# Optimization experiments

Measured on AMD Instinct MI355X. Metric: run time of the kernel, lower is better.

## Reference

```python
import jax, jax.numpy as jnp
import numpy as np

HEADS = 16
DIM_HEAD = 64
SCALE = DIM_HEAD ** -0.5
LN_EPS = 1e-5


def setup_inputs() -> dict:
    key = jax.random.key(0)
    ks = jax.random.split(key, 4)
    B, N, D = 2, 2048, 1024
    inner = HEADS * DIM_HEAD  # 1024
    x = jax.random.normal(ks[0], (B, N, D), dtype=jnp.float32)
    m = jax.random.normal(ks[1], (B, N, N), dtype=jnp.float32)
    gamma = jnp.ones((D,), dtype=jnp.float32)
    beta = jnp.zeros((D,), dtype=jnp.float32)
    W_qkv = jax.random.normal(ks[2], (D, 3 * inner), dtype=jnp.float32) * (D ** -0.5)
    W_out = jax.random.normal(ks[3], (inner, D), dtype=jnp.float32) * (inner ** -0.5)
    return {"x": x, "m": m, "gamma": gamma, "beta": beta, "W_qkv": W_qkv, "W_out": W_out}


def reference(x, m, gamma, beta, W_qkv, W_out):
    B, N, D = x.shape
    # LayerNorm
    mu = jnp.mean(x, axis=-1, keepdims=True)
    var = jnp.var(x, axis=-1, keepdims=True)
    xn = (x - mu) * jax.lax.rsqrt(var + LN_EPS) * gamma + beta
    # QKV projection (no bias)
    qkv = xn @ W_qkv  # [B, N, 3*inner]
    q, k, v = jnp.split(qkv, 3, axis=-1)
    split_heads = lambda t: t.reshape(B, N, HEADS, DIM_HEAD).transpose(0, 2, 1, 3)  # b h n d
    q, k, v = split_heads(q), split_heads(k), split_heads(v)
    # Non-standard order: mask added BEFORE scaling
    qk = jnp.einsum('bhid,bhjd->bhij', q, k)
    dots = (qk + m[:, None, :, :]) * SCALE
    attn = jax.nn.softmax(dots, axis=-1)
    out = jnp.einsum('bhij,bhjd->bhid', attn, v)
    out = out.transpose(0, 2, 1, 3).reshape(B, N, HEADS * DIM_HEAD)
    return out @ W_out  # dropout is identity at inference
```

## Files before the change

kernel.cpp:

```cpp
#include <hip/hip_runtime.h>
#include <hip/hip_bf16.h>
#include <math.h>

typedef _Float16 f16;
typedef _Float16 f16x4 __attribute__((ext_vector_type(4)));
typedef _Float16 f16x8 __attribute__((ext_vector_type(8)));
typedef float f32x4 __attribute__((ext_vector_type(4)));

#define HD 64
#define NH 16
#define BATCH 2
#define SEQ 2048
#define DMODEL 1024
#define NQKV 3072
#define ROWS 4096
#define NEG_BIG (-1.0e30f)
#define SCALE_LOG2E 0.18033688011112042f

__device__ __forceinline__ f32x4 mfma16h(f16x8 a, f16x8 b, f32x4 c){
  return __builtin_amdgcn_mfma_f32_16x16x32_f16(a, b, c, 0, 0, 0);
}

__device__ __forceinline__ void gload16(const f16* g, f16* l){
  __builtin_amdgcn_global_load_lds(
      (const __attribute__((address_space(1))) unsigned int*)(g),
      (__attribute__((address_space(3))) unsigned int*)(l), 16, 0, 0);
}

__global__ __launch_bounds__(256) void ln_kernel(const float* __restrict__ x,
    const float* __restrict__ gamma, const float* __restrict__ beta,
    f16* __restrict__ xn)
{
  int row = blockIdx.x;
  int tid = threadIdx.x;
  float4 v = ((const float4*)(x + (size_t)row * DMODEL))[tid];
  float s  = v.x + v.y + v.z + v.w;
  float s2 = v.x*v.x + v.y*v.y + v.z*v.z + v.w*v.w;
  #pragma unroll
  for (int off = 32; off; off >>= 1){ s += __shfl_xor(s, off); s2 += __shfl_xor(s2, off); }
  __shared__ float red[8];
  int wave = tid >> 6, lane = tid & 63;
  if (lane == 0){ red[wave] = s; red[4 + wave] = s2; }
  __syncthreads();
  s  = red[0] + red[1] + red[2] + red[3];
  s2 = red[4] + red[5] + red[6] + red[7];
  float mu  = s * (1.f / DMODEL);
  float var = s2 * (1.f / DMODEL) - mu * mu;
  float rs  = rsqrtf(var + 1e-5f);
  float4 g  = ((const float4*)gamma)[tid];
  float4 be = ((const float4*)beta)[tid];
  f16x4 o;
  o[0] = (f16)((v.x - mu) * rs * g.x + be.x);
  o[1] = (f16)((v.y - mu) * rs * g.y + be.y);
  o[2] = (f16)((v.z - mu) * rs * g.z + be.z);
  o[3] = (f16)((v.w - mu) * rs * g.w + be.w);
  *(f16x4*)(xn + (size_t)row * DMODEL + tid*4) = o;
}

__global__ __launch_bounds__(256) void transpose_f2h_kernel(const float* __restrict__ in,
    f16* __restrict__ out, int R, int C)
{
  __shared__ float t[32][33];
  int c0 = blockIdx.x * 32, r0 = blockIdx.y * 32;
  int lx = threadIdx.x & 31, ly = threadIdx.x >> 5;
  #pragma unroll
  for (int i = 0; i < 32; i += 8) t[ly + i][lx] = in[(size_t)(r0 + ly + i) * C + c0 + lx];
  __syncthreads();
  #pragma unroll
  for (int i = 0; i < 32; i += 8) out[(size_t)(c0 + ly + i) * R + r0 + lx] = (f16)t[lx][ly + i];
}

__global__ __launch_bounds__(256, 3) void gemm_qkv(const f16* __restrict__ A,
    const f16* __restrict__ Bt, f16* __restrict__ Qo, f16* __restrict__ Ko,
    f16* __restrict__ Vo)
{
  __shared__ __align__(16) f16 As[2][128][32];
  __shared__ __align__(16) f16 Bs[2][128][32];
  const int K = DMODEL;
  int bm = blockIdx.y * 128, bn = blockIdx.x * 128;
  int tid = threadIdx.x;
  int wave = tid >> 6, lane = tid & 63, quad = lane >> 4, l15 = lane & 15;
  int mw = (wave >> 1) * 64, nw = (wave & 1) * 64;

  int sr0 = wave*16 + (lane >> 2);
  int sr1 = sr0 + 64;
  int sc  = (lane & 3) ^ (sr0 & 3);
  const f16* Ag = A  + (size_t)bm * K;
  const f16* Bg = Bt + (size_t)bn * K;
  f16* ldsA0 = &As[0][wave*16     ][0];
  f16* ldsA1 = &As[0][wave*16 + 64][0];
  f16* ldsB0 = &Bs[0][wave*16     ][0];
  f16* ldsB1 = &Bs[0][wave*16 + 64][0];

#define QSTAGE(buf, k0) do{ \
    gload16(Ag + (size_t)sr0 * K + (k0) + sc*8, ldsA0 + (buf)*4096); \
    gload16(Ag + (size_t)sr1 * K + (k0) + sc*8, ldsA1 + (buf)*4096); \
    gload16(Bg + (size_t)sr0 * K + (k0) + sc*8, ldsB0 + (buf)*4096); \
    gload16(Bg + (size_t)sr1 * K + (k0) + sc*8, ldsB1 + (buf)*4096); }while(0)

  f32x4 zero = {0.f, 0.f, 0.f, 0.f};
  f32x4 acc[4][4];
  #pragma unroll
  for (int i = 0; i < 4; i++)
    #pragma unroll
    for (int j = 0; j < 4; j++) acc[i][j] = zero;

  QSTAGE(0, 0);
  const int NS = K / 32;
  for (int it = 0; it < NS; ++it){
    int cur = it & 1;
    asm volatile("s_waitcnt vmcnt(0)" ::: "memory");
    __syncthreads();
    if (it + 1 < NS) QSTAGE(cur ^ 1, (it + 1) * 32);
    int ca = (quad ^ (l15 & 3)) * 8;
    f16x8 af[4], bfr[4];
    #pragma unroll
    for (int i = 0; i < 4; i++) af[i]  = *(const f16x8*)&As[cur][mw + i*16 + l15][ca];
    #pragma unroll
    for (int i = 0; i < 4; i++) bfr[i] = *(const f16x8*)&Bs[cur][nw + i*16 + l15][ca];
    __builtin_amdgcn_s_setprio(1);
    #pragma unroll
    for (int mi = 0; mi < 4; mi++)
      #pragma unroll
      for (int ni = 0; ni < 4; ni++)
        acc[mi][ni] = mfma16h(af[mi], bfr[ni], acc[mi][ni]);
    __builtin_amdgcn_s_setprio(0);
  }
#undef QSTAGE

  #pragma unroll
  for (int mi = 0; mi < 4; mi++){
    #pragma unroll
    for (int ni = 0; ni < 4; ni++){
      int c = bn + nw + ni*16 + l15;
      int which = c >> 10;
      int hc = c & 1023;
      int h = hc >> 6, d = hc & 63;
      if (which == 2){
        int r = bm + mw + mi*16 + quad*4;
        int b = r >> 11, nseq = r & 2047;
        size_t bh = (size_t)(b * NH + h);
        f16x4 vv;
        #pragma unroll
        for (int reg = 0; reg < 4; reg++) vv[reg] = (f16)acc[mi][ni][reg];
        *(f16x4*)(Vo + (bh * HD + d) * SEQ + nseq) = vv;
      } else {
        #pragma unroll
        for (int reg = 0; reg < 4; reg++){
          int r = bm + mw + mi*16 + quad*4 + reg;
          float v = acc[mi][ni][reg];
          int b = r >> 11, nseq = r & 2047;
          size_t bh = (size_t)(b * NH + h);
          if (which == 0) Qo[(bh * SEQ + nseq) * HD + d] = (f16)v;
          else            Ko[(bh * SEQ + nseq) * HD + d] = (f16)v;
        }
      }
    }
  }
}

__global__ __launch_bounds__(256, 4) void gemm_out(const f16* __restrict__ A,
    const f16* __restrict__ Bt, float* __restrict__ C, int M, int N, int K)
{
  __shared__ __align__(16) f16 As[2][64][32];
  __shared__ __align__(16) f16 Bs[2][128][32];
  int bm = blockIdx.y * 64, bn = blockIdx.x * 128;
  int tid = threadIdx.x;
  int wave = tid >> 6, lane = tid & 63, quad = lane >> 4, l15 = lane & 15;
  int mw = (wave >> 1) * 32, nw = (wave & 1) * 64;

  int sr0 = wave*16 + (lane >> 2);
  int sc  = (lane & 3) ^ (sr0 & 3);
  const f16* Ag = A  + (size_t)bm * K;
  const f16* Bg = Bt + (size_t)bn * K;
  f16* ldsA0 = &As[0][wave*16     ][0];
  f16* ldsB0 = &Bs[0][wave*16     ][0];
  f16* ldsB1 = &Bs[0][wave*16 + 64][0];

#define OSTAGE(buf, k0) do{ \
    gload16(Ag + (size_t)sr0 * K + (k0) + sc*8, ldsA0 + (buf)*2048); \
    gload16(Bg + (size_t)sr0 * K + (k0) + sc*8, ldsB0 + (buf)*4096); \
    gload16(Bg + (size_t)(sr0 + 64) * K + (k0) + sc*8, ldsB1 + (buf)*4096); }while(0)

  f32x4 zero = {0.f, 0.f, 0.f, 0.f};
  f32x4 acc[2][4];
  #pragma unroll
  for (int i = 0; i < 2; i++)
    #pragma unroll
    for (int j = 0; j < 4; j++) acc[i][j] = zero;

  OSTAGE(0, 0);
  const int NS = DMODEL / 32;
  for (int it = 0; it < NS; ++it){
    int cur = it & 1;
    asm volatile("s_waitcnt vmcnt(0)" ::: "memory");
    __syncthreads();
    if (it + 1 < NS) OSTAGE(cur ^ 1, (it + 1) * 32);
    int ca = (quad ^ (l15 & 3)) * 8;
    f16x8 af[2], bfr[4];
    #pragma unroll
    for (int i = 0; i < 2; i++) af[i]  = *(const f16x8*)&As[cur][mw + i*16 + l15][ca];
    #pragma unroll
    for (int i = 0; i < 4; i++) bfr[i] = *(const f16x8*)&Bs[cur][nw + i*16 + l15][ca];
    __builtin_amdgcn_s_setprio(1);
    #pragma unroll
    for (int mi = 0; mi < 2; mi++)
      #pragma unroll
      for (int ni = 0; ni < 4; ni++)
        acc[mi][ni] = mfma16h(af[mi], bfr[ni], acc[mi][ni]);
    __builtin_amdgcn_s_setprio(0);
  }
#undef OSTAGE

  #pragma unroll
  for (int mi = 0; mi < 2; mi++)
    #pragma unroll
    for (int ni = 0; ni < 4; ni++)
      #pragma unroll
      for (int reg = 0; reg < 4; reg++){
        int r = bm + mw + mi*16 + quad*4 + reg;
        int c = bn + nw + ni*16 + l15;
        C[(size_t)r * N + c] = acc[mi][ni][reg];
      }
}

__global__ __launch_bounds__(256, 4) void attn_kernel(const f16* __restrict__ Q,
    const f16* __restrict__ Kb, const f16* __restrict__ Vt,
    const float* __restrict__ mask, f16* __restrict__ Ao)
{
  __shared__ __align__(16) f16 KsB[2][64*64];
  __shared__ __align__(16) f16 VsB[2][64*64];
  __shared__ __align__(16) f16 Ps[4*16*64];

  int bh = blockIdx.y; int b = bh >> 4; int h = bh & 15;
  int q0 = blockIdx.x * 64;
  int tid = threadIdx.x;
  int wave = tid >> 6, lane = tid & 63, quad = lane >> 4, l15 = lane & 15;

  int rA = (wave*2 + 0)*8 + (lane >> 3);
  int rB = (wave*2 + 1)*8 + (lane >> 3);
  int cp = lane & 7;
  int ccA = cp ^ (rA & 7);
  int ccB = cp ^ (rB & 7);
  const f16* Kg = Kb + (size_t)bh * SEQ * HD;
  const f16* Vg = Vt + (size_t)bh * HD * SEQ;
  f16* ldsKA = &KsB[0][0] + (wave*2 + 0)*8*64;
  f16* ldsKB = &KsB[0][0] + (wave*2 + 1)*8*64;
  f16* ldsVA = &VsB[0][0] + (wave*2 + 0)*8*64;
  f16* ldsVB = &VsB[0][0] + (wave*2 + 1)*8*64;

  f16x8 qf[2];
  {
    const f16* qrow = Q + ((size_t)bh * SEQ + q0 + wave*16 + l15) * HD + quad*8;
    qf[0] = *(const f16x8*)(qrow);
    qf[1] = *(const f16x8*)(qrow + 32);
  }

  const float* mrow = mask + ((size_t)b * SEQ + q0 + wave*16 + l15) * SEQ + quad*4;

  gload16(Kg + (size_t)(0 + rA)*HD + ccA*8, ldsKA);
  gload16(Kg + (size_t)(0 + rB)*HD + ccB*8, ldsKB);
  gload16(Vg + (size_t)rA*SEQ + 0 + ccA*8, ldsVA);
  gload16(Vg + (size_t)rB*SEQ + 0 + ccB*8, ldsVB);

  f32x4 zero = {0.f, 0.f, 0.f, 0.f};
  f32x4 O[4];
  #pragma unroll
  for (int nt = 0; nt < 4; nt++) O[nt] = zero;
  float mrun = NEG_BIG, lrun = 0.f;

  const int NT = SEQ / 64;
  for (int it = 0; it < NT; ++it){
    int cur = it & 1;
    int j0 = it * 64;
    asm volatile("s_waitcnt vmcnt(0)" ::: "memory");
    __syncthreads();
    if (it + 1 < NT){
      int nb = cur ^ 1;
      int j0n = j0 + 64;
      gload16(Kg + (size_t)(j0n + rA)*HD + ccA*8, ldsKA + nb*4096);
      gload16(Kg + (size_t)(j0n + rB)*HD + ccB*8, ldsKB + nb*4096);
      gload16(Vg + (size_t)rA*SEQ + j0n + ccA*8, ldsVA + nb*4096);
      gload16(Vg + (size_t)rB*SEQ + j0n + ccB*8, ldsVB + nb*4096);
    }
    const f16* Ksc = &KsB[cur][0];
    const f16* Vsc = &VsB[cur][0];

    float sv[4][4];
    __builtin_amdgcn_s_setprio(1);
    #pragma unroll
    for (int jt = 0; jt < 4; jt++){
      f32x4 a = zero;
      int r = jt*16 + l15;
      #pragma unroll
      for (int kk = 0; kk < 2; kk++){
        f16x8 kf = *(const f16x8*)&Ksc[r*64 + (((kk*4 + quad) ^ (r & 7))*8)];
        a = mfma16h(kf, qf[kk], a);
      }
      float4 mv = *(const float4*)(mrow + j0 + jt*16);
      sv[jt][0] = (a[0] + mv.x) * SCALE_LOG2E;
      sv[jt][1] = (a[1] + mv.y) * SCALE_LOG2E;
      sv[jt][2] = (a[2] + mv.z) * SCALE_LOG2E;
      sv[jt][3] = (a[3] + mv.w) * SCALE_LOG2E;
    }
    __builtin_amdgcn_s_setprio(0);

    float m0 = fmaxf(fmaxf(sv[0][0], sv[0][1]), fmaxf(sv[0][2], sv[0][3]));
    float m1 = fmaxf(fmaxf(sv[1][0], sv[1][1]), fmaxf(sv[1][2], sv[1][3]));
    float m2 = fmaxf(fmaxf(sv[2][0], sv[2][1]), fmaxf(sv[2][2], sv[2][3]));
    float m3 = fmaxf(fmaxf(sv[3][0], sv[3][1]), fmaxf(sv[3][2], sv[3][3]));
    float tmax = fmaxf(fmaxf(m0, m1), fmaxf(m2, m3));
    tmax = fmaxf(tmax, __shfl_xor(tmax, 16));
    tmax = fmaxf(tmax, __shfl_xor(tmax, 32));

    if (__any(tmax > mrun + 8.f)){
      float nm = fmaxf(mrun, tmax);
      float alpha = exp2f(mrun - nm);
      mrun = nm;
      lrun *= alpha;
      float aR[4];
      #pragma unroll
      for (int reg = 0; reg < 4; reg++)
        aR[reg] = __shfl(alpha, (lane & 48) | (quad*4 + reg));
      #pragma unroll
      for (int nt = 0; nt < 4; nt++)
        #pragma unroll
        for (int reg = 0; reg < 4; reg++) O[nt][reg] *= aR[reg];
    }

    float ps = 0.f;
    #pragma unroll
    for (int jt = 0; jt < 4; jt++)
      #pragma unroll
      for (int reg = 0; reg < 4; reg++){
        float p = exp2f(sv[jt][reg] - mrun);
        sv[jt][reg] = p; ps += p;
      }
    lrun += ps;

    #pragma unroll
    for (int jt = 0; jt < 4; jt++){
      f16x4 ph;
      ph[0] = (f16)sv[jt][0]; ph[1] = (f16)sv[jt][1];
      ph[2] = (f16)sv[jt][2]; ph[3] = (f16)sv[jt][3];
      *(f16x4*)&Ps[wave*1024 + l15*64 + (((jt*2 + (quad>>1)) ^ (l15 & 7))*8) + (quad & 1)*4] = ph;
    }

    __builtin_amdgcn_s_setprio(1);
    #pragma unroll
    for (int nt = 0; nt < 4; nt++){
      #pragma unroll
      for (int kk = 0; kk < 2; kk++){
        int rv = nt*16 + l15;
        f16x8 pf = *(const f16x8*)&Ps[wave*1024 + l15*64 + (((kk*4 + quad) ^ (l15 & 7))*8)];
        f16x8 vf = *(const f16x8*)&Vsc[rv*64 + (((kk*4 + quad) ^ (rv & 7))*8)];
        O[nt] = mfma16h(pf, vf, O[nt]);
      }
    }
    __builtin_amdgcn_s_setprio(0);
  }

  lrun += __shfl_xor(lrun, 16);
  lrun += __shfl_xor(lrun, 32);
  float lR[4];
  #pragma unroll
  for (int reg = 0; reg < 4; reg++)
    lR[reg] = __shfl(lrun, (lane & 48) | (quad*4 + reg));
  #pragma unroll
  for (int nt = 0; nt < 4; nt++){
    #pragma unroll
    for (int reg = 0; reg < 4; reg++){
      float o = O[nt][reg] / lR[reg];
      int r = q0 + wave*16 + quad*4 + reg;
      Ao[((size_t)(b * SEQ + r)) * DMODEL + h * HD + nt*16 + l15] = (f16)o;
    }
  }
}

extern "C" void kernel_launch(void* const* d_in, const int* in_sizes, int n_in,
                              void* d_out, int out_size, void* d_ws, size_t ws_size,
                              hipStream_t stream)
{
  (void)in_sizes; (void)n_in; (void)out_size; (void)ws_size;
  const float* x     = (const float*)d_in[0];
  const float* m     = (const float*)d_in[1];
  const float* gamma = (const float*)d_in[2];
  const float* beta  = (const float*)d_in[3];
  const float* Wqkv  = (const float*)d_in[4];
  const float* Wout  = (const float*)d_in[5];
  float* out = (float*)d_out;

  char* ws = (char*)d_ws;
  f16* xn    = (f16*)(ws + 0);
  f16* Ao    = (f16*)(ws + 0);
  f16* Qb    = (f16*)(ws + 8388608);
  f16* WoutT = (f16*)(ws + 8388608);
  f16* Kbuf  = (f16*)(ws + 16777216);
  f16* Vtb   = (f16*)(ws + 25165824);
  f16* WqkvT = (f16*)(ws + 33554432);

  ln_kernel<<<ROWS, 256, 0, stream>>>(x, gamma, beta, xn);
  transpose_f2h_kernel<<<dim3(NQKV/32, DMODEL/32), 256, 0, stream>>>(Wqkv, WqkvT, DMODEL, NQKV);
  gemm_qkv<<<dim3(NQKV/128, ROWS/128), 256, 0, stream>>>(xn, WqkvT, Qb, Kbuf, Vtb);
  attn_kernel<<<dim3(SEQ/64, BATCH*NH), 256, 0, stream>>>(Qb, Kbuf, Vtb, m, Ao);
  transpose_f2h_kernel<<<dim3(DMODEL/32, DMODEL/32), 256, 0, stream>>>(Wout, WoutT, DMODEL, DMODEL);
  gemm_out<<<dim3(DMODEL/128, ROWS/64), 256, 0, stream>>>(Ao, WoutT, out, ROWS, DMODEL, DMODEL);
}
```

Before: 253.1 us.

## Process 128 query rows per attention block, two 16-row tiles per wave

Each wave now handles two 16-row query tiles, so the block covers 128 queries and the grid halves. K and V fragments loaded from LDS are reused across both tiles, which halves K/V global and LDS traffic per query. The mask loads are hoisted ahead of the QK MFMAs. In exchange, register pressure roughly doubles (launch bounds lowered to 2 blocks per CU), the grid shrinks to 512 blocks, and occupancy drops.

```diff
diff --git a/kernel.cpp b/kernel.cpp
--- a/kernel.cpp
+++ b/kernel.cpp
@@ -224,16 +224,16 @@
       }
 }
 
-__global__ __launch_bounds__(256, 4) void attn_kernel(const f16* __restrict__ Q,
+__global__ __launch_bounds__(256, 2) void attn_kernel(const f16* __restrict__ Q,
     const f16* __restrict__ Kb, const f16* __restrict__ Vt,
     const float* __restrict__ mask, f16* __restrict__ Ao)
 {
   __shared__ __align__(16) f16 KsB[2][64*64];
   __shared__ __align__(16) f16 VsB[2][64*64];
-  __shared__ __align__(16) f16 Ps[4*16*64];
+  __shared__ __align__(16) f16 Ps[8*16*64];
 
   int bh = blockIdx.y; int b = bh >> 4; int h = bh & 15;
-  int q0 = blockIdx.x * 64;
+  int q0 = blockIdx.x * 128;
   int tid = threadIdx.x;
   int wave = tid >> 6, lane = tid & 63, quad = lane >> 4, l15 = lane & 15;
 
@@ -249,14 +249,18 @@
   f16* ldsVA = &VsB[0][0] + (wave*2 + 0)*8*64;
   f16* ldsVB = &VsB[0][0] + (wave*2 + 1)*8*64;
 
-  f16x8 qf[2];
-  {
-    const f16* qrow = Q + ((size_t)bh * SEQ + q0 + wave*16 + l15) * HD + quad*8;
-    qf[0] = *(const f16x8*)(qrow);
-    qf[1] = *(const f16x8*)(qrow + 32);
-  }
-
-  const float* mrow = mask + ((size_t)b * SEQ + q0 + wave*16 + l15) * SEQ + quad*4;
+  f16x8 qf[2][2];
+  #pragma unroll
+  for (int u = 0; u < 2; u++){
+    const f16* qrow = Q + ((size_t)bh * SEQ + q0 + wave*32 + u*16 + l15) * HD + quad*8;
+    qf[u][0] = *(const f16x8*)(qrow);
+    qf[u][1] = *(const f16x8*)(qrow + 32);
+  }
+
+  const float* mrow[2];
+  #pragma unroll
+  for (int u = 0; u < 2; u++)
+    mrow[u] = mask + ((size_t)b * SEQ + q0 + wave*32 + u*16 + l15) * SEQ + quad*4;
 
   gload16(Kg + (size_t)(0 + rA)*HD + ccA*8, ldsKA);
   gload16(Kg + (size_t)(0 + rB)*HD + ccB*8, ldsKB);
@@ -264,10 +268,12 @@
   gload16(Vg + (size_t)rB*SEQ + 0 + ccB*8, ldsVB);
 
   f32x4 zero = {0.f, 0.f, 0.f, 0.f};
-  f32x4 O[4];
-  #pragma unroll
-  for (int nt = 0; nt < 4; nt++) O[nt] = zero;
-  float mrun = NEG_BIG, lrun = 0.f;
+  f32x4 O[2][4];
+  #pragma unroll
+  for (int u = 0; u < 2; u++)
+    #pragma unroll
+    for (int nt = 0; nt < 4; nt++) O[u][nt] = zero;
+  float mrun[2] = {NEG_BIG, NEG_BIG}, lrun[2] = {0.f, 0.f};
 
   const int NT = SEQ / 64;
   for (int it = 0; it < NT; ++it){
@@ -286,93 +292,117 @@
     const f16* Ksc = &KsB[cur][0];
     const f16* Vsc = &VsB[cur][0];
 
-    float sv[4][4];
+    float4 mc[2][4];
+    #pragma unroll
+    for (int u = 0; u < 2; u++)
+      #pragma unroll
+      for (int jt = 0; jt < 4; jt++)
+        mc[u][jt] = *(const float4*)(mrow[u] + j0 + jt*16);
+
+    float sv[2][4][4];
     __builtin_amdgcn_s_setprio(1);
     #pragma unroll
     for (int jt = 0; jt < 4; jt++){
-      f32x4 a = zero;
       int r = jt*16 + l15;
-      #pragma unroll
-      for (int kk = 0; kk < 2; kk++){
-        f16x8 kf = *(const f16x8*)&Ksc[r*64 + (((kk*4 + quad) ^ (r & 7))*8)];
-        a = mfma16h(kf, qf[kk], a);
-      }
-      float4 mv = *(const float4*)(mrow + j0 + jt*16);
-      sv[jt][0] = (a[0] + mv.x) * SCALE_LOG2E;
-      sv[jt][1] = (a[1] + mv.y) * SCALE_LOG2E;
-      sv[jt][2] = (a[2] + mv.z) * SCALE_LOG2E;
-      sv[jt][3] = (a[3] + mv.w) * SCALE_LOG2E;
+      f16x8 kf0 = *(const f16x8*)&Ksc[r*64 + (((0 + quad) ^ (r & 7))*8)];
+      f16x8 kf1 = *(const f16x8*)&Ksc[r*64 + (((4 + quad) ^ (r & 7))*8)];
+      #pragma unroll
+      for (int u = 0; u < 2; u++){
+        f32x4 a = zero;
+        a = mfma16h(kf0, qf[u][0], a);
+        a = mfma16h(kf1, qf[u][1], a);
+        sv[u][jt][0] = (a[0] + mc[u][jt].x) * SCALE_LOG2E;
+        sv[u][jt][1] = (a[1] + mc[u][jt].y) * SCALE_LOG2E;
+        sv[u][jt][2] = (a[2] + mc[u][jt].z) * SCALE_LOG2E;
+        sv[u][jt][3] = (a[3] + mc[u][jt].w) * SCALE_LOG2E;
+      }
     }
     __builtin_amdgcn_s_setprio(0);
 
-    float m0 = fmaxf(fmaxf(sv[0][0], sv[0][1]), fmaxf(sv[0][2], sv[0][3]));
-    float m1 = fmaxf(fmaxf(sv[1][0], sv[1][1]), fmaxf(sv[1][2], sv[1][3]));
-    float m2 = fmaxf(fmaxf(sv[2][0], sv[2][1]), fmaxf(sv[2][2], sv[2][3]));
-    float m3 = fmaxf(fmaxf(sv[3][0], sv[3][1]), fmaxf(sv[3][2], sv[3][3]));
-    float tmax = fmaxf(fmaxf(m0, m1), fmaxf(m2, m3));
-    tmax = fmaxf(tmax, __shfl_xor(tmax, 16));
-    tmax = fmaxf(tmax, __shfl_xor(tmax, 32));
-
-    if (__any(tmax > mrun + 8.f)){
-      float nm = fmaxf(mrun, tmax);
-      float alpha = exp2f(mrun - nm);
-      mrun = nm;
-      lrun *= alpha;
-      float aR[4];
-      #pragma unroll
-      for (int reg = 0; reg < 4; reg++)
-        aR[reg] = __shfl(alpha, (lane & 48) | (quad*4 + reg));
-      #pragma unroll
-      for (int nt = 0; nt < 4; nt++)
+    #pragma unroll
+    for (int u = 0; u < 2; u++){
+      float m0 = fmaxf(fmaxf(sv[u][0][0], sv[u][0][1]), fmaxf(sv[u][0][2], sv[u][0][3]));
+      float m1 = fmaxf(fmaxf(sv[u][1][0], sv[u][1][1]), fmaxf(sv[u][1][2], sv[u][1][3]));
+      float m2 = fmaxf(fmaxf(sv[u][2][0], sv[u][2][1]), fmaxf(sv[u][2][2], sv[u][2][3]));
+      float m3 = fmaxf(fmaxf(sv[u][3][0], sv[u][3][1]), fmaxf(sv[u][3][2], sv[u][3][3]));
+      float tmax = fmaxf(fmaxf(m0, m1), fmaxf(m2, m3));
+      tmax = fmaxf(tmax, __shfl_xor(tmax, 16));
+      tmax = fmaxf(tmax, __shfl_xor(tmax, 32));
+
+      if (__any(tmax > mrun[u] + 8.f)){
+        float nm = fmaxf(mrun[u], tmax);
+        float alpha = exp2f(mrun[u] - nm);
+        mrun[u] = nm;
+        lrun[u] *= alpha;
+        float aR[4];
         #pragma unroll
-        for (int reg = 0; reg < 4; reg++) O[nt][reg] *= aR[reg];
-    }
-
-    float ps = 0.f;
-    #pragma unroll
-    for (int jt = 0; jt < 4; jt++)
+        for (int reg = 0; reg < 4; reg++)
+          aR[reg] = __shfl(alpha, (lane & 48) | (quad*4 + reg));
+        #pragma unroll
+        for (int nt = 0; nt < 4; nt++)
+          #pragma unroll
+          for (int reg = 0; reg < 4; reg++) O[u][nt][reg] *= aR[reg];
+      }
+
+      float ps = 0.f;
+      #pragma unroll
+      for (int jt = 0; jt < 4; jt++)
+        #pragma unroll
+        for (int reg = 0; reg < 4; reg++){
+          float p = exp2f(sv[u][jt][reg] - mrun[u]);
+          sv[u][jt][reg] = p; ps += p;
+        }
+      lrun[u] += ps;
+
+      #pragma unroll
+      for (int jt = 0; jt < 4; jt++){
+        f16x4 ph;
+        ph[0] = (f16)sv[u][jt][0]; ph[1] = (f16)sv[u][jt][1];
+        ph[2] = (f16)sv[u][jt][2]; ph[3] = (f16)sv[u][jt][3];
+        *(f16x4*)&Ps[wave*2048 + u*1024 + l15*64
+                     + (((jt*2 + (quad>>1)) ^ (l15 & 7))*8) + (quad & 1)*4] = ph;
+      }
+    }
+
+    f16x8 pf[2][2];
+    #pragma unroll
+    for (int u = 0; u < 2; u++)
+      #pragma unroll
+      for (int kk = 0; kk < 2; kk++)
+        pf[u][kk] = *(const f16x8*)&Ps[wave*2048 + u*1024 + l15*64
+                                       + (((kk*4 + quad) ^ (l15 & 7))*8)];
+    __builtin_amdgcn_s_setprio(1);
+    #pragma unroll
+    for (int nt = 0; nt < 4; nt++){
+      int rv = nt*16 + l15;
+      f16x8 vf0 = *(const f16x8*)&Vsc[rv*64 + (((0 + quad) ^ (rv & 7))*8)];
+      f16x8 vf1 = *(const f16x8*)&Vsc[rv*64 + (((4 + quad) ^ (rv & 7))*8)];
+      #pragma unroll
+      for (int u = 0; u < 2; u++){
+        O[u][nt] = mfma16h(pf[u][0], vf0, O[u][nt]);
+        O[u][nt] = mfma16h(pf[u][1], vf1, O[u][nt]);
+      }
+    }
+    __builtin_amdgcn_s_setprio(0);
+  }
+
+  #pragma unroll
+  for (int u = 0; u < 2; u++){
+    float l = lrun[u];
+    l += __shfl_xor(l, 16);
+    l += __shfl_xor(l, 32);
+    float lR[4];
+    #pragma unroll
+    for (int reg = 0; reg < 4; reg++)
+      lR[reg] = __shfl(l, (lane & 48) | (quad*4 + reg));
+    #pragma unroll
+    for (int nt = 0; nt < 4; nt++){
       #pragma unroll
       for (int reg = 0; reg < 4; reg++){
-        float p = exp2f(sv[jt][reg] - mrun);
-        sv[jt][reg] = p; ps += p;
-      }
-    lrun += ps;
-
-    #pragma unroll
-    for (int jt = 0; jt < 4; jt++){
-      f16x4 ph;
-      ph[0] = (f16)sv[jt][0]; ph[1] = (f16)sv[jt][1];
-      ph[2] = (f16)sv[jt][2]; ph[3] = (f16)sv[jt][3];
-      *(f16x4*)&Ps[wave*1024 + l15*64 + (((jt*2 + (quad>>1)) ^ (l15 & 7))*8) + (quad & 1)*4] = ph;
-    }
-
-    __builtin_amdgcn_s_setprio(1);
-    #pragma unroll
-    for (int nt = 0; nt < 4; nt++){
-      #pragma unroll
-      for (int kk = 0; kk < 2; kk++){
-        int rv = nt*16 + l15;
-        f16x8 pf = *(const f16x8*)&Ps[wave*1024 + l15*64 + (((kk*4 + quad) ^ (l15 & 7))*8)];
-        f16x8 vf = *(const f16x8*)&Vsc[rv*64 + (((kk*4 + quad) ^ (rv & 7))*8)];
-        O[nt] = mfma16h(pf, vf, O[nt]);
-      }
-    }
-    __builtin_amdgcn_s_setprio(0);
-  }
-
-  lrun += __shfl_xor(lrun, 16);
-  lrun += __shfl_xor(lrun, 32);
-  float lR[4];
-  #pragma unroll
-  for (int reg = 0; reg < 4; reg++)
-    lR[reg] = __shfl(lrun, (lane & 48) | (quad*4 + reg));
-  #pragma unroll
-  for (int nt = 0; nt < 4; nt++){
-    #pragma unroll
-    for (int reg = 0; reg < 4; reg++){
-      float o = O[nt][reg] / lR[reg];
-      int r = q0 + wave*16 + quad*4 + reg;
-      Ao[((size_t)(b * SEQ + r)) * DMODEL + h * HD + nt*16 + l15] = (f16)o;
+        float o = O[u][nt][reg] / lR[reg];
+        int r = q0 + wave*32 + u*16 + quad*4 + reg;
+        Ao[((size_t)(b * SEQ + r)) * DMODEL + h * HD + nt*16 + l15] = (f16)o;
+      }
     }
   }
 }
@@ -402,7 +432,7 @@
   ln_kernel<<<ROWS, 256, 0, stream>>>(x, gamma, beta, xn);
   transpose_f2h_kernel<<<dim3(NQKV/32, DMODEL/32), 256, 0, stream>>>(Wqkv, WqkvT, DMODEL, NQKV);
   gemm_qkv<<<dim3(NQKV/128, ROWS/128), 256, 0, stream>>>(xn, WqkvT, Qb, Kbuf, Vtb);
-  attn_kernel<<<dim3(SEQ/64, BATCH*NH), 256, 0, stream>>>(Qb, Kbuf, Vtb, m, Ao);
+  attn_kernel<<<dim3(SEQ/128, BATCH*NH), 256, 0, stream>>>(Qb, Kbuf, Vtb, m, Ao);
   transpose_f2h_kernel<<<dim3(DMODEL/32, DMODEL/32), 256, 0, stream>>>(Wout, WoutT, DMODEL, DMODEL);
   gemm_out<<<dim3(DMODEL/128, ROWS/64), 256, 0, stream>>>(Ao, WoutT, out, ROWS, DMODEL, DMODEL);
 }
```

Result: slower. 258.5 us (+2.2%).

## Rewrite attention with 32x32 MFMA tiles, register-resident P via permlane swap

Applied to the files above, without the earlier changes.

The attention kernel now processes 128 query rows per block (32 per wave) using 32x32x16 MFMA instructions. The softmax probabilities are repacked in registers with permlane32_swap instead of a round trip through LDS. The softmax scale is folded into Q inside the QKV GEMM epilogue, so only the mask needs an FMA with the scale. The output is staged through an LDS slab so global stores are 16-byte and coalesced. This halves the grid and raises register use (launch bound lowered to 2 blocks per CU), which risks lower occupancy in exchange for more reuse of each K/V tile.

```diff
diff --git a/kernel.cpp b/kernel.cpp
--- a/kernel.cpp
+++ b/kernel.cpp
@@ -3,9 +3,12 @@
 #include <math.h>
 
 typedef _Float16 f16;
+typedef __fp16 hf2 __attribute__((ext_vector_type(2)));
 typedef _Float16 f16x4 __attribute__((ext_vector_type(4)));
 typedef _Float16 f16x8 __attribute__((ext_vector_type(8)));
 typedef float f32x4 __attribute__((ext_vector_type(4)));
+typedef float f32x16 __attribute__((ext_vector_type(16)));
+typedef unsigned int u32x2 __attribute__((ext_vector_type(2)));
 
 #define HD 64
 #define NH 16
@@ -19,6 +22,16 @@
 
 __device__ __forceinline__ f32x4 mfma16h(f16x8 a, f16x8 b, f32x4 c){
   return __builtin_amdgcn_mfma_f32_16x16x32_f16(a, b, c, 0, 0, 0);
+}
+__device__ __forceinline__ f32x16 mfma32h(f16x8 a, f16x8 b, f32x16 c){
+  return __builtin_amdgcn_mfma_f32_32x32x16_f16(a, b, c, 0, 0, 0);
+}
+__device__ __forceinline__ u32x2 pswap(unsigned a, unsigned b){
+  return __builtin_amdgcn_permlane32_swap(a, b, false, false);
+}
+__device__ __forceinline__ unsigned pk16(float a, float b){
+  hf2 r = __builtin_amdgcn_cvt_pkrtz(a, b);
+  return __builtin_bit_cast(unsigned, r);
 }
 
 __device__ __forceinline__ void gload16(const f16* g, f16* l){
@@ -151,7 +164,7 @@
           float v = acc[mi][ni][reg];
           int b = r >> 11, nseq = r & 2047;
           size_t bh = (size_t)(b * NH + h);
-          if (which == 0) Qo[(bh * SEQ + nseq) * HD + d] = (f16)v;
+          if (which == 0) Qo[(bh * SEQ + nseq) * HD + d] = (f16)(v * SCALE_LOG2E);
           else            Ko[(bh * SEQ + nseq) * HD + d] = (f16)v;
         }
       }
@@ -224,18 +237,19 @@
       }
 }
 
-__global__ __launch_bounds__(256, 4) void attn_kernel(const f16* __restrict__ Q,
+__global__ __launch_bounds__(256, 2) void attn_kernel(const f16* __restrict__ Q,
     const f16* __restrict__ Kb, const f16* __restrict__ Vt,
     const float* __restrict__ mask, f16* __restrict__ Ao)
 {
   __shared__ __align__(16) f16 KsB[2][64*64];
   __shared__ __align__(16) f16 VsB[2][64*64];
-  __shared__ __align__(16) f16 Ps[4*16*64];
+  __shared__ __align__(16) f16 Ob[4][32*72];
 
   int bh = blockIdx.y; int b = bh >> 4; int h = bh & 15;
-  int q0 = blockIdx.x * 64;
+  int q0 = blockIdx.x * 128;
   int tid = threadIdx.x;
-  int wave = tid >> 6, lane = tid & 63, quad = lane >> 4, l15 = lane & 15;
+  int wave = tid >> 6, lane = tid & 63;
+  int l31 = lane & 31, hi = lane >> 5;
 
   int rA = (wave*2 + 0)*8 + (lane >> 3);
   int rB = (wave*2 + 1)*8 + (lane >> 3);
@@ -249,24 +263,23 @@
   f16* ldsVA = &VsB[0][0] + (wave*2 + 0)*8*64;
   f16* ldsVB = &VsB[0][0] + (wave*2 + 1)*8*64;
 
-  f16x8 qf[2];
+  f16x8 qb[4];
   {
-    const f16* qrow = Q + ((size_t)bh * SEQ + q0 + wave*16 + l15) * HD + quad*8;
-    qf[0] = *(const f16x8*)(qrow);
-    qf[1] = *(const f16x8*)(qrow + 32);
-  }
-
-  const float* mrow = mask + ((size_t)b * SEQ + q0 + wave*16 + l15) * SEQ + quad*4;
+    const f16* qrow = Q + ((size_t)bh * SEQ + q0 + wave*32 + l31) * HD + hi*8;
+    #pragma unroll
+    for (int kt = 0; kt < 4; kt++) qb[kt] = *(const f16x8*)(qrow + kt*16);
+  }
+
+  const float* mrow = mask + ((size_t)b * SEQ + q0 + wave*32 + l31) * SEQ;
 
   gload16(Kg + (size_t)(0 + rA)*HD + ccA*8, ldsKA);
   gload16(Kg + (size_t)(0 + rB)*HD + ccB*8, ldsKB);
   gload16(Vg + (size_t)rA*SEQ + 0 + ccA*8, ldsVA);
   gload16(Vg + (size_t)rB*SEQ + 0 + ccB*8, ldsVB);
 
-  f32x4 zero = {0.f, 0.f, 0.f, 0.f};
-  f32x4 O[4];
-  #pragma unroll
-  for (int nt = 0; nt < 4; nt++) O[nt] = zero;
+  f32x16 O0, O1;
+  #pragma unroll
+  for (int i = 0; i < 16; i++){ O0[i] = 0.f; O1[i] = 0.f; }
   float mrun = NEG_BIG, lrun = 0.f;
 
   const int NT = SEQ / 64;
@@ -286,94 +299,129 @@
     const f16* Ksc = &KsB[cur][0];
     const f16* Vsc = &VsB[cur][0];
 
-    float sv[4][4];
+    float4 mv0[4], mv1[4];
+    #pragma unroll
+    for (int g = 0; g < 4; g++){
+      mv0[g] = *(const float4*)(mrow + j0 +      g*8 + hi*4);
+      mv1[g] = *(const float4*)(mrow + j0 + 32 + g*8 + hi*4);
+    }
+
+    f32x16 s0, s1;
+    #pragma unroll
+    for (int i = 0; i < 16; i++){ s0[i] = 0.f; s1[i] = 0.f; }
     __builtin_amdgcn_s_setprio(1);
     #pragma unroll
-    for (int jt = 0; jt < 4; jt++){
-      f32x4 a = zero;
-      int r = jt*16 + l15;
-      #pragma unroll
-      for (int kk = 0; kk < 2; kk++){
-        f16x8 kf = *(const f16x8*)&Ksc[r*64 + (((kk*4 + quad) ^ (r & 7))*8)];
-        a = mfma16h(kf, qf[kk], a);
-      }
-      float4 mv = *(const float4*)(mrow + j0 + jt*16);
-      sv[jt][0] = (a[0] + mv.x) * SCALE_LOG2E;
-      sv[jt][1] = (a[1] + mv.y) * SCALE_LOG2E;
-      sv[jt][2] = (a[2] + mv.z) * SCALE_LOG2E;
-      sv[jt][3] = (a[3] + mv.w) * SCALE_LOG2E;
+    for (int kt = 0; kt < 4; kt++){
+      int c = ((kt*2 + hi) ^ (l31 & 7)) * 8;
+      f16x8 ka0 = *(const f16x8*)&Ksc[ l31      *64 + c];
+      f16x8 ka1 = *(const f16x8*)&Ksc[(32 + l31)*64 + c];
+      s0 = mfma32h(ka0, qb[kt], s0);
+      s1 = mfma32h(ka1, qb[kt], s1);
     }
     __builtin_amdgcn_s_setprio(0);
 
-    float m0 = fmaxf(fmaxf(sv[0][0], sv[0][1]), fmaxf(sv[0][2], sv[0][3]));
-    float m1 = fmaxf(fmaxf(sv[1][0], sv[1][1]), fmaxf(sv[1][2], sv[1][3]));
-    float m2 = fmaxf(fmaxf(sv[2][0], sv[2][1]), fmaxf(sv[2][2], sv[2][3]));
-    float m3 = fmaxf(fmaxf(sv[3][0], sv[3][1]), fmaxf(sv[3][2], sv[3][3]));
-    float tmax = fmaxf(fmaxf(m0, m1), fmaxf(m2, m3));
-    tmax = fmaxf(tmax, __shfl_xor(tmax, 16));
-    tmax = fmaxf(tmax, __shfl_xor(tmax, 32));
+    float p0[16], p1[16];
+    #pragma unroll
+    for (int g = 0; g < 4; g++){
+      p0[g*4+0] = fmaf(mv0[g].x, SCALE_LOG2E, s0[g*4+0]);
+      p0[g*4+1] = fmaf(mv0[g].y, SCALE_LOG2E, s0[g*4+1]);
+      p0[g*4+2] = fmaf(mv0[g].z, SCALE_LOG2E, s0[g*4+2]);
+      p0[g*4+3] = fmaf(mv0[g].w, SCALE_LOG2E, s0[g*4+3]);
+      p1[g*4+0] = fmaf(mv1[g].x, SCALE_LOG2E, s1[g*4+0]);
+      p1[g*4+1] = fmaf(mv1[g].y, SCALE_LOG2E, s1[g*4+1]);
+      p1[g*4+2] = fmaf(mv1[g].z, SCALE_LOG2E, s1[g*4+2]);
+      p1[g*4+3] = fmaf(mv1[g].w, SCALE_LOG2E, s1[g*4+3]);
+    }
+
+    float t0 = fmaxf(fmaxf(fmaxf(p0[0],p0[1]),fmaxf(p0[2],p0[3])),
+                     fmaxf(fmaxf(p0[4],p0[5]),fmaxf(p0[6],p0[7])));
+    float t1 = fmaxf(fmaxf(fmaxf(p0[8],p0[9]),fmaxf(p0[10],p0[11])),
+                     fmaxf(fmaxf(p0[12],p0[13]),fmaxf(p0[14],p0[15])));
+    float t2 = fmaxf(fmaxf(fmaxf(p1[0],p1[1]),fmaxf(p1[2],p1[3])),
+                     fmaxf(fmaxf(p1[4],p1[5]),fmaxf(p1[6],p1[7])));
+    float t3 = fmaxf(fmaxf(fmaxf(p1[8],p1[9]),fmaxf(p1[10],p1[11])),
+                     fmaxf(fmaxf(p1[12],p1[13]),fmaxf(p1[14],p1[15])));
+    float tmax = fmaxf(fmaxf(t0, t1), fmaxf(t2, t3));
+    {
+      u32x2 r = pswap(__float_as_uint(tmax), __float_as_uint(tmax));
+      tmax = fmaxf(__uint_as_float(r[0]), __uint_as_float(r[1]));
+    }
 
     if (__any(tmax > mrun + 8.f)){
       float nm = fmaxf(mrun, tmax);
       float alpha = exp2f(mrun - nm);
       mrun = nm;
       lrun *= alpha;
-      float aR[4];
       #pragma unroll
-      for (int reg = 0; reg < 4; reg++)
-        aR[reg] = __shfl(alpha, (lane & 48) | (quad*4 + reg));
-      #pragma unroll
-      for (int nt = 0; nt < 4; nt++)
-        #pragma unroll
-        for (int reg = 0; reg < 4; reg++) O[nt][reg] *= aR[reg];
+      for (int i = 0; i < 16; i++){ O0[i] *= alpha; O1[i] *= alpha; }
     }
 
     float ps = 0.f;
     #pragma unroll
-    for (int jt = 0; jt < 4; jt++)
-      #pragma unroll
-      for (int reg = 0; reg < 4; reg++){
-        float p = exp2f(sv[jt][reg] - mrun);
-        sv[jt][reg] = p; ps += p;
-      }
+    for (int i = 0; i < 16; i++){
+      p0[i] = exp2f(p0[i] - mrun); ps += p0[i];
+      p1[i] = exp2f(p1[i] - mrun); ps += p1[i];
+    }
     lrun += ps;
 
+    unsigned u0[4][2], u1[4][2];
+    #pragma unroll
+    for (int g = 0; g < 4; g++){
+      u0[g][0] = pk16(p0[g*4+0], p0[g*4+1]);
+      u0[g][1] = pk16(p0[g*4+2], p0[g*4+3]);
+      u1[g][0] = pk16(p1[g*4+0], p1[g*4+1]);
+      u1[g][1] = pk16(p1[g*4+2], p1[g*4+3]);
+    }
+    f16x8 pb[4];
+    #pragma unroll
+    for (int m = 0; m < 2; m++){
+      u32x2 r0 = pswap(u0[2*m][0], u0[2*m+1][0]);
+      u32x2 r1 = pswap(u0[2*m][1], u0[2*m+1][1]);
+      union { unsigned u[4]; f16x8 v; } w;
+      w.u[0] = r0[0]; w.u[1] = r1[0]; w.u[2] = r0[1]; w.u[3] = r1[1];
+      pb[m] = w.v;
+      r0 = pswap(u1[2*m][0], u1[2*m+1][0]);
+      r1 = pswap(u1[2*m][1], u1[2*m+1][1]);
+      w.u[0] = r0[0]; w.u[1] = r1[0]; w.u[2] = r0[1]; w.u[3] = r1[1];
+      pb[2 + m] = w.v;
+    }
+
+    __builtin_amdgcn_s_setprio(1);
     #pragma unroll
     for (int jt = 0; jt < 4; jt++){
-      f16x4 ph;
-      ph[0] = (f16)sv[jt][0]; ph[1] = (f16)sv[jt][1];
-      ph[2] = (f16)sv[jt][2]; ph[3] = (f16)sv[jt][3];
-      *(f16x4*)&Ps[wave*1024 + l15*64 + (((jt*2 + (quad>>1)) ^ (l15 & 7))*8) + (quad & 1)*4] = ph;
-    }
-
-    __builtin_amdgcn_s_setprio(1);
-    #pragma unroll
-    for (int nt = 0; nt < 4; nt++){
-      #pragma unroll
-      for (int kk = 0; kk < 2; kk++){
-        int rv = nt*16 + l15;
-        f16x8 pf = *(const f16x8*)&Ps[wave*1024 + l15*64 + (((kk*4 + quad) ^ (l15 & 7))*8)];
-        f16x8 vf = *(const f16x8*)&Vsc[rv*64 + (((kk*4 + quad) ^ (rv & 7))*8)];
-        O[nt] = mfma16h(pf, vf, O[nt]);
-      }
+      int c = ((jt*2 + hi) ^ (l31 & 7)) * 8;
+      f16x8 va0 = *(const f16x8*)&Vsc[ l31      *64 + c];
+      f16x8 va1 = *(const f16x8*)&Vsc[(32 + l31)*64 + c];
+      O0 = mfma32h(va0, pb[jt], O0);
+      O1 = mfma32h(va1, pb[jt], O1);
     }
     __builtin_amdgcn_s_setprio(0);
   }
 
-  lrun += __shfl_xor(lrun, 16);
-  lrun += __shfl_xor(lrun, 32);
-  float lR[4];
-  #pragma unroll
-  for (int reg = 0; reg < 4; reg++)
-    lR[reg] = __shfl(lrun, (lane & 48) | (quad*4 + reg));
-  #pragma unroll
-  for (int nt = 0; nt < 4; nt++){
-    #pragma unroll
-    for (int reg = 0; reg < 4; reg++){
-      float o = O[nt][reg] / lR[reg];
-      int r = q0 + wave*16 + quad*4 + reg;
-      Ao[((size_t)(b * SEQ + r)) * DMODEL + h * HD + nt*16 + l15] = (f16)o;
-    }
+  {
+    u32x2 r = pswap(__float_as_uint(lrun), __float_as_uint(lrun));
+    lrun = __uint_as_float(r[0]) + __uint_as_float(r[1]);
+  }
+  float inv = 1.0f / lrun;
+  f16* slab = &Ob[wave][0];
+  #pragma unroll
+  for (int g = 0; g < 4; g++){
+    f16x4 w0, w1;
+    #pragma unroll
+    for (int rg = 0; rg < 4; rg++){
+      w0[rg] = (f16)(O0[g*4+rg] * inv);
+      w1[rg] = (f16)(O1[g*4+rg] * inv);
+    }
+    *(f16x4*)&slab[l31*72 +      g*8 + hi*4] = w0;
+    *(f16x4*)&slab[l31*72 + 32 + g*8 + hi*4] = w1;
+  }
+  int ir  = lane >> 3;
+  int c16 = lane & 7;
+  #pragma unroll
+  for (int rr = 0; rr < 4; rr++){
+    int i = rr*8 + ir;
+    f16x8 ov = *(const f16x8*)&slab[i*72 + c16*8];
+    *(f16x8*)(Ao + ((size_t)(b * SEQ + q0 + wave*32 + i)) * DMODEL + h * HD + c16*8) = ov;
   }
 }
 
@@ -402,7 +450,7 @@
   ln_kernel<<<ROWS, 256, 0, stream>>>(x, gamma, beta, xn);
   transpose_f2h_kernel<<<dim3(NQKV/32, DMODEL/32), 256, 0, stream>>>(Wqkv, WqkvT, DMODEL, NQKV);
   gemm_qkv<<<dim3(NQKV/128, ROWS/128), 256, 0, stream>>>(xn, WqkvT, Qb, Kbuf, Vtb);
-  attn_kernel<<<dim3(SEQ/64, BATCH*NH), 256, 0, stream>>>(Qb, Kbuf, Vtb, m, Ao);
+  attn_kernel<<<dim3(SEQ/128, BATCH*NH), 256, 0, stream>>>(Qb, Kbuf, Vtb, m, Ao);
   transpose_f2h_kernel<<<dim3(DMODEL/32, DMODEL/32), 256, 0, stream>>>(Wout, WoutT, DMODEL, DMODEL);
   gemm_out<<<dim3(DMODEL/128, ROWS/64), 256, 0, stream>>>(Ao, WoutT, out, ROWS, DMODEL, DMODEL);
 }
```

New measurement: 256.7 us. About the same (+1.4%).
